# Kernel tuning notes

Hardware: AMD Instinct MI355X
Metric: run time of the kernel (lower is better)

Reference implementation:

```python
import jax, jax.numpy as jnp
import numpy as np

B, S, D, H = 2, 2048, 2048, 16
HD = D // H  # head_dim = 128


def setup_inputs() -> dict:
    key = jax.random.key(0)
    ks = jax.random.split(key, 9)
    std = 0.02
    x = jax.random.normal(ks[0], (B, S, D), dtype=jnp.float32)
    Wq = jax.random.normal(ks[1], (D, D), dtype=jnp.float32) * std
    bq = jnp.zeros((D,), dtype=jnp.float32)
    Wk = jax.random.normal(ks[2], (D, D), dtype=jnp.float32) * std
    bk = jnp.zeros((D,), dtype=jnp.float32)
    Wv = jax.random.normal(ks[3], (D, D), dtype=jnp.float32) * std
    bv = jnp.zeros((D,), dtype=jnp.float32)
    Wo = jax.random.normal(ks[4], (D, D), dtype=jnp.float32) * std
    bo = jnp.zeros((D,), dtype=jnp.float32)
    return {"x": x, "Wq": Wq, "bq": bq, "Wk": Wk, "bk": bk,
            "Wv": Wv, "bv": bv, "Wo": Wo, "bo": bo}


def _rope_tables(seq_len, head_dim, base=10000.0):
    # inv_freq over even indices; freqs: [S, HD/2]
    inv_freq = 1.0 / (base ** (jnp.arange(0, head_dim, 2, dtype=jnp.float32) / head_dim))
    t = jnp.arange(seq_len, dtype=jnp.float32)
    freqs = jnp.einsum('i,j->ij', t, inv_freq)
    return jnp.cos(freqs), jnp.sin(freqs)  # each [S, HD/2]


def _rotate(x, cos, sin):
    # x: [B, H, S, HD]; cos/sin: [S, HD/2] broadcast over B,H
    x1, x2 = jnp.split(x, 2, axis=-1)
    return jnp.concatenate([x1 * cos - x2 * sin, x1 * sin + x2 * cos], axis=-1)


def reference(x, Wq, bq, Wk, bk, Wv, bv, Wo, bo):
    b, s, d = x.shape
    q = (jnp.einsum('bsd,df->bsf', x, Wq) + bq).reshape(b, s, H, HD).transpose(0, 2, 1, 3)
    k = (jnp.einsum('bsd,df->bsf', x, Wk) + bk).reshape(b, s, H, HD).transpose(0, 2, 1, 3)
    v = (jnp.einsum('bsd,df->bsf', x, Wv) + bv).reshape(b, s, H, HD).transpose(0, 2, 1, 3)
    cos, sin = _rope_tables(s, HD)
    qr = _rotate(q, cos, sin)
    kr = _rotate(k, cos, sin)
    scores = jnp.einsum('bhqd,bhkd->bhqk', qr, kr) / jnp.sqrt(jnp.float32(HD))
    probs = jax.nn.softmax(scores, axis=-1)
    out = jnp.einsum('bhqk,bhkd->bhqd', probs, v)
    out = out.transpose(0, 2, 1, 3).reshape(b, s, d)
    return jnp.einsum('bsd,df->bsf', out, Wo) + bo
```

## Files before the change

kernel.cpp:

```cpp
#include <hip/hip_runtime.h>

#define BB  2
#define SS  2048
#define DD  2048
#define HH  16
#define HDD 128
#define BSR 4096

using short8  = __attribute__((ext_vector_type(8))) short;
using floatx4 = __attribute__((ext_vector_type(4))) float;

__device__ __forceinline__ float bf2f(unsigned short u) {
  return __uint_as_float(((unsigned int)u) << 16);
}
__device__ __forceinline__ unsigned short f2bf(float f) {
  unsigned int u = __float_as_uint(f);
  u += 0x7fffu + ((u >> 16) & 1u);
  return (unsigned short)(u >> 16);
}
__device__ __forceinline__ unsigned int pk2bf(float a, float b) {
  unsigned int ua = __float_as_uint(a);
  ua += 0x7fffu + ((ua >> 16) & 1u);
  unsigned int ub = __float_as_uint(b);
  ub += 0x7fffu + ((ub >> 16) & 1u);
  return (ua >> 16) | (ub & 0xffff0000u);
}
__device__ __forceinline__ void gl_lds16(const void* g, void* l) {
  __builtin_amdgcn_global_load_lds(
      (__attribute__((address_space(1))) void*)g,
      (__attribute__((address_space(3))) void*)l, 16, 0, 0);
}

__global__ __launch_bounds__(256) void transpose_w(
    const float* __restrict__ Wq, const float* __restrict__ Wk,
    const float* __restrict__ Wv, const float* __restrict__ Wo,
    unsigned short* __restrict__ wqkvt, unsigned short* __restrict__ wot)
{
  __shared__ float tile[32][33];
  const float* W; unsigned short* Out;
  int z = blockIdx.z;
  if      (z == 0) { W = Wq; Out = wqkvt; }
  else if (z == 1) { W = Wk; Out = wqkvt + (size_t)DD * DD; }
  else if (z == 2) { W = Wv; Out = wqkvt + 2 * (size_t)DD * DD; }
  else             { W = Wo; Out = wot; }
  int tx = threadIdx.x, ty = threadIdx.y;
  int d0 = blockIdx.y * 32, f0 = blockIdx.x * 32;
#pragma unroll
  for (int i = 0; i < 4; i++)
    tile[ty + i * 8][tx] = W[(size_t)(d0 + ty + i * 8) * DD + f0 + tx];
  __syncthreads();
#pragma unroll
  for (int i = 0; i < 4; i++)
    Out[(size_t)(f0 + ty + i * 8) * DD + d0 + tx] = f2bf(tile[tx][ty + i * 8]);
}

__global__ __launch_bounds__(256) void conv_x(const float* __restrict__ x,
                                              unsigned short* __restrict__ xb)
{
  size_t i = ((size_t)blockIdx.x * 256 + threadIdx.x) * 4;
  float4 v = *(const float4*)(x + i);
  ushort4 o;
  o.x = f2bf(v.x); o.y = f2bf(v.y); o.z = f2bf(v.z); o.w = f2bf(v.w);
  *(ushort4*)(xb + i) = o;
}

template <bool OUTF32>
__global__ __launch_bounds__(256) void gemm_bt(
    const unsigned short* __restrict__ A, const unsigned short* __restrict__ Bt,
    const float* __restrict__ bias, void* __restrict__ Cout,
    int M, int N, int K)
{
  __shared__ unsigned short As[128 * 64];
  __shared__ unsigned short Bs[128 * 64];
  int t = threadIdx.x;
  int m0 = blockIdx.y * 128, n0 = blockIdx.x * 128;
  int w = t >> 6, lane = t & 63, qd = lane >> 4, l16 = lane & 15;
  int wm = (w >> 1) * 64, wn = (w & 1) * 64;
  floatx4 zero4 = {0.f, 0.f, 0.f, 0.f};
  floatx4 acc[4][4];
#pragma unroll
  for (int i = 0; i < 4; i++)
#pragma unroll
    for (int j = 0; j < 4; j++) acc[i][j] = zero4;

  int gchunk = (t & 7) ^ ((t >> 3) & 7);
  const unsigned short* Ab = A  + (size_t)(m0 + (t >> 3)) * K + gchunk * 8;
  const unsigned short* Bb = Bt + (size_t)(n0 + (t >> 3)) * K + gchunk * 8;
  size_t qK = (size_t)32 * K;

  for (int k0 = 0; k0 < K; k0 += 64) {
    __syncthreads();
#pragma unroll
    for (int c = 0; c < 4; c++) {
      gl_lds16(Ab + c * qK + k0, &As[(c * 256 + t) * 8]);
      gl_lds16(Bb + c * qK + k0, &Bs[(c * 256 + t) * 8]);
    }
    __syncthreads();
#pragma unroll
    for (int ks = 0; ks < 2; ks++) {
      int ch = ((ks * 4 + qd) ^ (l16 & 7)) * 8;
      short8 af[4], bfr[4];
#pragma unroll
      for (int i = 0; i < 4; i++)
        af[i] = *(const short8*)&As[(wm + i * 16 + l16) * 64 + ch];
#pragma unroll
      for (int j = 0; j < 4; j++)
        bfr[j] = *(const short8*)&Bs[(wn + j * 16 + l16) * 64 + ch];
#pragma unroll
      for (int i = 0; i < 4; i++)
#pragma unroll
        for (int j = 0; j < 4; j++)
          acc[i][j] = __builtin_amdgcn_mfma_f32_16x16x32_bf16(af[i], bfr[j], acc[i][j], 0, 0, 0);
    }
  }

#pragma unroll
  for (int i = 0; i < 4; i++)
#pragma unroll
    for (int j = 0; j < 4; j++) {
      int row = m0 + wm + i * 16 + qd * 4;
      int col = n0 + wn + j * 16 + l16;
      float bsv = bias ? bias[col] : 0.f;
#pragma unroll
      for (int r = 0; r < 4; r++) {
        float v = acc[i][j][r] + bsv;
        if (OUTF32) ((float*)Cout)[(size_t)(row + r) * N + col] = v;
        else ((unsigned short*)Cout)[(size_t)(row + r) * N + col] = f2bf(v);
      }
    }
}

__global__ __launch_bounds__(256) void rope_qk(
    const unsigned short* __restrict__ qkv, const float* __restrict__ bq,
    const float* __restrict__ bk, unsigned short* __restrict__ q_r,
    unsigned short* __restrict__ k_r)
{
  int lin = blockIdx.x * 256 + threadIdx.x;
  int i = lin & 63;
  int s = (lin >> 6) & (SS - 1);
  int h = (lin >> 17) & (HH - 1);
  int b = lin >> 21;
  size_t row = (size_t)(b * SS + s) * (3 * DD);
  int f = h * HDD + i;
  float q1 = bf2f(qkv[row + f])            + bq[f];
  float q2 = bf2f(qkv[row + f + 64])       + bq[f + 64];
  float k1 = bf2f(qkv[row + DD + f])       + bk[f];
  float k2 = bf2f(qkv[row + DD + f + 64])  + bk[f + 64];
  float inv = powf(10000.f, -(float)i * (1.f / 64.f));
  float ang = (float)s * inv;
  float sn, c;
  sincosf(ang, &sn, &c);
  const float qs = 0.08838834764831845f;
  size_t ob = ((size_t)(b * HH + h) * SS + s) * HDD;
  q_r[ob + i]      = f2bf((q1 * c - q2 * sn) * qs);
  q_r[ob + i + 64] = f2bf((q1 * sn + q2 * c) * qs);
  k_r[ob + i]      = f2bf(k1 * c - k2 * sn);
  k_r[ob + i + 64] = f2bf(k1 * sn + k2 * c);
}

__global__ __launch_bounds__(256) void v_transpose(
    const unsigned short* __restrict__ qkv, const float* __restrict__ bv,
    unsigned short* __restrict__ v_t)
{
  __shared__ float tile[32][33];
  int bh = blockIdx.z; int b = bh >> 4, h = bh & 15;
  int s0 = blockIdx.x * 32, d0 = blockIdx.y * 32;
  int tx = threadIdx.x, ty = threadIdx.y;
#pragma unroll
  for (int i = 0; i < 4; i++) {
    int s = s0 + ty + i * 8, dh = d0 + tx;
    tile[ty + i * 8][tx] =
        bf2f(qkv[(size_t)(b * SS + s) * (3 * DD) + 2 * DD + h * HDD + dh]) + bv[h * HDD + dh];
  }
  __syncthreads();
  int s = s0 + tx;
  int y = s & 63;
  int kap = ((y >> 5) & 1) * 32 + ((y >> 2) & 3) * 8 + ((y >> 4) & 1) * 4 + (y & 3);
  int scol = (s & ~63) + kap;
#pragma unroll
  for (int i = 0; i < 4; i++)
    v_t[((size_t)(b * HH + h) * HDD + d0 + ty + i * 8) * SS + scol] =
        f2bf(tile[tx][ty + i * 8]);
}

__global__ __launch_bounds__(256, 2) void attn_kernel(
    const unsigned short* __restrict__ q_r, const unsigned short* __restrict__ k_r,
    const unsigned short* __restrict__ v_t, unsigned short* __restrict__ aout)
{
  __shared__ unsigned short Ks[2][64 * 128];
  __shared__ unsigned short Vs[2][128 * 64];
  int t = threadIdx.x, w = t >> 6, lane = t & 63, qd = lane >> 4, l16 = lane & 15;
  int L = blockIdx.y * gridDim.x + blockIdx.x;
  int jj = L >> 3;
  int bh = (L & 7) * 4 + (jj >> 4);
  int q0 = (jj & 15) * 128;
  const unsigned short* qb = q_r + (size_t)bh * SS * HDD;
  const unsigned short* kb = k_r + (size_t)bh * SS * HDD;
  const unsigned short* vb = v_t + (size_t)bh * HDD * SS;

  short8 aq[2][4];
#pragma unroll
  for (int mi = 0; mi < 2; mi++)
#pragma unroll
    for (int ks = 0; ks < 4; ks++)
      aq[mi][ks] = *(const short8*)
          &qb[(size_t)(q0 + w * 32 + mi * 16 + l16) * HDD + ks * 32 + qd * 8];

  float m_i[2], l_i[2];
  floatx4 zero4 = {0.f, 0.f, 0.f, 0.f};
  floatx4 o[2][8];
#pragma unroll
  for (int mi = 0; mi < 2; mi++) { m_i[mi] = -1e30f; l_i[mi] = 0.f; }
#pragma unroll
  for (int mi = 0; mi < 2; mi++)
#pragma unroll
    for (int n = 0; n < 8; n++) o[mi][n] = zero4;

  auto stage = [&](int nb, int kt) {
#pragma unroll
    for (int c = 0; c < 4; c++) {
      int flat = c * 256 + t;
      int r = flat >> 4, cc = flat & 15;
      gl_lds16(kb + (size_t)(kt + r) * HDD + (cc ^ (r & 15)) * 8, &Ks[nb][flat * 8]);
    }
#pragma unroll
    for (int c = 0; c < 4; c++) {
      int flat = c * 256 + t;
      int r = flat >> 3, cc = flat & 7;
      gl_lds16(vb + (size_t)r * SS + kt + (cc ^ (r & 7)) * 8, &Vs[nb][flat * 8]);
    }
  };

  stage(0, 0);
  int buf = 0;

  for (int kt = 0; kt < SS; kt += 64) {
    __syncthreads();
    if (kt + 64 < SS) stage(buf ^ 1, kt + 64);

    floatx4 sc[2][4];
#pragma unroll
    for (int mi = 0; mi < 2; mi++)
#pragma unroll
      for (int j = 0; j < 4; j++) sc[mi][j] = zero4;
#pragma unroll
    for (int j = 0; j < 4; j++) {
      int krow = j * 16 + l16;
#pragma unroll
      for (int ks = 0; ks < 4; ks++) {
        int chunk = ks * 4 + qd;
        short8 kf = *(const short8*)&Ks[buf][krow * 128 + ((chunk ^ (krow & 15)) * 8)];
        sc[0][j] = __builtin_amdgcn_mfma_f32_16x16x32_bf16(kf, aq[0][ks], sc[0][j], 0, 0, 0);
        sc[1][j] = __builtin_amdgcn_mfma_f32_16x16x32_bf16(kf, aq[1][ks], sc[1][j], 0, 0, 0);
      }
    }

    float rmax[2];
#pragma unroll
    for (int mi = 0; mi < 2; mi++) {
      float m = sc[mi][0][0];
#pragma unroll
      for (int j = 0; j < 4; j++)
#pragma unroll
        for (int r = 0; r < 4; r++) m = fmaxf(m, sc[mi][j][r]);
      m = fmaxf(m, __shfl_xor(m, 16, 64));
      m = fmaxf(m, __shfl_xor(m, 32, 64));
      rmax[mi] = m;
    }

    bool up = (rmax[0] > m_i[0]) || (rmax[1] > m_i[1]);
    if (__ballot(up) != 0ull) {
#pragma unroll
      for (int mi = 0; mi < 2; mi++) {
        float mn = fmaxf(m_i[mi], rmax[mi]);
        float a = __expf(m_i[mi] - mn);
        m_i[mi] = mn;
        l_i[mi] *= a;
#pragma unroll
        for (int n = 0; n < 8; n++)
#pragma unroll
          for (int r = 0; r < 4; r++) o[mi][n][r] *= a;
      }
    }

    unsigned int pr[2][4][2];
#pragma unroll
    for (int mi = 0; mi < 2; mi++) {
      float s0 = 0.f;
#pragma unroll
      for (int j = 0; j < 4; j++) {
        float p0 = __expf(sc[mi][j][0] - m_i[mi]);
        float p1 = __expf(sc[mi][j][1] - m_i[mi]);
        float p2 = __expf(sc[mi][j][2] - m_i[mi]);
        float p3 = __expf(sc[mi][j][3] - m_i[mi]);
        s0 += (p0 + p1) + (p2 + p3);
        pr[mi][j][0] = pk2bf(p0, p1);
        pr[mi][j][1] = pk2bf(p2, p3);
      }
      s0 += __shfl_xor(s0, 16, 64);
      s0 += __shfl_xor(s0, 32, 64);
      l_i[mi] += s0;
    }

#pragma unroll
    for (int n = 0; n < 8; n++) {
      int vrow = n * 16 + l16;
#pragma unroll
      for (int ks = 0; ks < 2; ks++) {
        int chunk = ks * 4 + qd;
        short8 av = *(const short8*)&Vs[buf][vrow * 64 + ((chunk ^ (vrow & 7)) * 8)];
        union { unsigned int u[4]; short8 v; } bp0, bp1;
        bp0.u[0] = pr[0][2 * ks][0];     bp0.u[1] = pr[0][2 * ks][1];
        bp0.u[2] = pr[0][2 * ks + 1][0]; bp0.u[3] = pr[0][2 * ks + 1][1];
        bp1.u[0] = pr[1][2 * ks][0];     bp1.u[1] = pr[1][2 * ks][1];
        bp1.u[2] = pr[1][2 * ks + 1][0]; bp1.u[3] = pr[1][2 * ks + 1][1];
        o[0][n] = __builtin_amdgcn_mfma_f32_16x16x32_bf16(av, bp0.v, o[0][n], 0, 0, 0);
        o[1][n] = __builtin_amdgcn_mfma_f32_16x16x32_bf16(av, bp1.v, o[1][n], 0, 0, 0);
      }
    }
    buf ^= 1;
  }

  int b = bh >> 4, h = bh & 15;
#pragma unroll
  for (int mi = 0; mi < 2; mi++) {
    int qrow = q0 + w * 32 + mi * 16 + l16;
    float inv_l = 1.f / l_i[mi];
    size_t base = ((size_t)(b * SS + qrow)) * DD + h * HDD;
#pragma unroll
    for (int n = 0; n < 8; n++) {
      uint2 pkd;
      pkd.x = pk2bf(o[mi][n][0] * inv_l, o[mi][n][1] * inv_l);
      pkd.y = pk2bf(o[mi][n][2] * inv_l, o[mi][n][3] * inv_l);
      *(uint2*)&aout[base + n * 16 + qd * 4] = pkd;
    }
  }
}

extern "C" void kernel_launch(void* const* d_in, const int* in_sizes, int n_in,
                              void* d_out, int out_size, void* d_ws, size_t ws_size,
                              hipStream_t stream) {
  const float* x  = (const float*)d_in[0];
  const float* Wq = (const float*)d_in[1];
  const float* bq = (const float*)d_in[2];
  const float* Wk = (const float*)d_in[3];
  const float* bk = (const float*)d_in[4];
  const float* Wv = (const float*)d_in[5];
  const float* bv = (const float*)d_in[6];
  const float* Wo = (const float*)d_in[7];
  const float* bo = (const float*)d_in[8];
  float* out = (float*)d_out;

  char* ws = (char*)d_ws;
  unsigned short* xb      = (unsigned short*)(ws + 0);
  unsigned short* wqkvt   = (unsigned short*)(ws + 16777216);
  unsigned short* wot     = (unsigned short*)(ws + 41943040);
  unsigned short* qkv     = (unsigned short*)(ws + 50331648);
  unsigned short* q_r     = (unsigned short*)(ws + 100663296);
  unsigned short* k_r     = (unsigned short*)(ws + 117440512);
  unsigned short* v_t     = (unsigned short*)(ws + 134217728);
  unsigned short* attn_o  = xb;

  transpose_w<<<dim3(DD / 32, DD / 32, 4), dim3(32, 8), 0, stream>>>(
      Wq, Wk, Wv, Wo, wqkvt, wot);
  conv_x<<<dim3((BSR * DD) / 1024), dim3(256), 0, stream>>>(x, xb);
  gemm_bt<false><<<dim3(3 * DD / 128, BSR / 128), dim3(256), 0, stream>>>(
      xb, wqkvt, nullptr, qkv, BSR, 3 * DD, DD);
  rope_qk<<<dim3((BB * HH * SS * 64) / 256), dim3(256), 0, stream>>>(
      qkv, bq, bk, q_r, k_r);
  v_transpose<<<dim3(SS / 32, HDD / 32, BB * HH), dim3(32, 8), 0, stream>>>(
      qkv, bv, v_t);
  attn_kernel<<<dim3(SS / 128, BB * HH), dim3(256), 0, stream>>>(
      q_r, k_r, v_t, attn_o);
  gemm_bt<true><<<dim3(DD / 128, BSR / 128), dim3(256), 0, stream>>>(
      attn_o, wot, bo, out, BSR, DD, DD);
}
```

Measured before the change: 443.7 us.

## Fuse bias, RoPE and V transpose into QKV GEMM epilogue; use exp2 in softmax

Adds a gemm_qkv kernel whose epilogue stages the output tile in LDS, adds the bias, applies RoPE from a precomputed cos/sin table, and writes Q/K in head-major layout and V transposed. This removes the bf16 qkv intermediate round-trip and the separate rope_qk and v_transpose kernels. The Q scale is changed to fold log2(e), and the attention softmax uses the native exp2 builtin instead of __expf, which saves a multiply per exponent. The fused epilogue adds LDS traffic and a bf16 rounding step before RoPE, and it depends on the log2e folding being consistent.

```diff
diff --git a/kernel.cpp b/kernel.cpp
--- a/kernel.cpp
+++ b/kernel.cpp
@@ -24,6 +24,13 @@
   unsigned int ub = __float_as_uint(b);
   ub += 0x7fffu + ((ub >> 16) & 1u);
   return (ua >> 16) | (ub & 0xffff0000u);
+}
+__device__ __forceinline__ float fexp2(float x) {
+#if __has_builtin(__builtin_amdgcn_exp2f)
+  return __builtin_amdgcn_exp2f(x);
+#else
+  return __expf(x * 0.6931471805599453f);
+#endif
 }
 __device__ __forceinline__ void gl_lds16(const void* g, void* l) {
   __builtin_amdgcn_global_load_lds(
@@ -64,6 +71,124 @@
   *(ushort4*)(xb + i) = o;
 }
 
+__global__ __launch_bounds__(256) void rope_tab(float2* __restrict__ rtab) {
+  int idx = blockIdx.x * 256 + threadIdx.x;
+  int s = idx >> 6, c = idx & 63;
+  float inv = powf(10000.f, -(float)c * (1.f / 64.f));
+  float ang = (float)s * inv;
+  float sn, cc;
+  sincosf(ang, &sn, &cc);
+  rtab[idx] = make_float2(cc, sn);
+}
+
+__global__ __launch_bounds__(256) void gemm_qkv(
+    const unsigned short* __restrict__ A, const unsigned short* __restrict__ Bt,
+    const float* __restrict__ bq, const float* __restrict__ bk,
+    const float* __restrict__ bv, const float2* __restrict__ rtab,
+    unsigned short* __restrict__ q_r, unsigned short* __restrict__ k_r,
+    unsigned short* __restrict__ v_t)
+{
+  __shared__ unsigned short smem[16896];
+  unsigned short* As = smem;
+  unsigned short* Bs = smem + 8192;
+  const int K = DD;
+  int t = threadIdx.x;
+  int m0 = blockIdx.y * 128, n0 = blockIdx.x * 128;
+  int w = t >> 6, lane = t & 63, qd = lane >> 4, l16 = lane & 15;
+  int wm = (w >> 1) * 64, wn = (w & 1) * 64;
+  floatx4 zero4 = {0.f, 0.f, 0.f, 0.f};
+  floatx4 acc[4][4];
+#pragma unroll
+  for (int i = 0; i < 4; i++)
+#pragma unroll
+    for (int j = 0; j < 4; j++) acc[i][j] = zero4;
+
+  int gchunk = (t & 7) ^ ((t >> 3) & 7);
+  const unsigned short* Ab = A  + (size_t)(m0 + (t >> 3)) * K + gchunk * 8;
+  const unsigned short* Bb = Bt + (size_t)(n0 + (t >> 3)) * K + gchunk * 8;
+  size_t qK = (size_t)32 * K;
+
+  for (int k0 = 0; k0 < K; k0 += 64) {
+    __syncthreads();
+#pragma unroll
+    for (int c = 0; c < 4; c++) {
+      gl_lds16(Ab + c * qK + k0, &As[(c * 256 + t) * 8]);
+      gl_lds16(Bb + c * qK + k0, &Bs[(c * 256 + t) * 8]);
+    }
+    __syncthreads();
+#pragma unroll
+    for (int ks = 0; ks < 2; ks++) {
+      int ch = ((ks * 4 + qd) ^ (l16 & 7)) * 8;
+      short8 af[4], bfr[4];
+#pragma unroll
+      for (int i = 0; i < 4; i++)
+        af[i] = *(const short8*)&As[(wm + i * 16 + l16) * 64 + ch];
+#pragma unroll
+      for (int j = 0; j < 4; j++)
+        bfr[j] = *(const short8*)&Bs[(wn + j * 16 + l16) * 64 + ch];
+#pragma unroll
+      for (int i = 0; i < 4; i++)
+#pragma unroll
+        for (int j = 0; j < 4; j++)
+          acc[i][j] = __builtin_amdgcn_mfma_f32_16x16x32_bf16(af[i], bfr[j], acc[i][j], 0, 0, 0);
+    }
+  }
+
+  int plane = n0 >> 11;
+  int h = (n0 >> 7) & 15;
+  const float* bias = plane == 0 ? bq : (plane == 1 ? bk : bv);
+  __syncthreads();
+#pragma unroll
+  for (int i = 0; i < 4; i++)
+#pragma unroll
+    for (int j = 0; j < 4; j++) {
+      int rl = wm + i * 16 + qd * 4;
+      int cl = wn + j * 16 + l16;
+      float bsv = bias[h * 128 + cl];
+#pragma unroll
+      for (int r = 0; r < 4; r++)
+        smem[(rl + r) * 132 + cl] = f2bf(acc[i][j][r] + bsv);
+    }
+  __syncthreads();
+
+  int b = m0 >> 11, sbase = m0 & (SS - 1);
+  if (plane < 2) {
+    unsigned short* dst = (plane == 0 ? q_r : k_r) + (size_t)(b * HH + h) * SS * HDD;
+    const float fac = (plane == 0) ? 0.12751744f : 1.0f;
+#pragma unroll
+    for (int it = 0; it < 16; it++) {
+      int idx = it * 256 + t;
+      int rl = idx >> 5, c2 = (idx & 31) * 2;
+      int s = sbase + rl;
+      float4 cs = *(const float4*)&rtab[(size_t)s * 64 + c2];
+      float a0 = bf2f(smem[rl * 132 + c2]);
+      float a1 = bf2f(smem[rl * 132 + c2 + 1]);
+      float b0 = bf2f(smem[rl * 132 + c2 + 64]);
+      float b1 = bf2f(smem[rl * 132 + c2 + 65]);
+      unsigned int lo = pk2bf((a0 * cs.x - b0 * cs.y) * fac,
+                              (a1 * cs.z - b1 * cs.w) * fac);
+      unsigned int hi = pk2bf((a0 * cs.y + b0 * cs.x) * fac,
+                              (a1 * cs.w + b1 * cs.z) * fac);
+      size_t rowb = (size_t)s * HDD;
+      *(unsigned int*)&dst[rowb + c2]      = lo;
+      *(unsigned int*)&dst[rowb + c2 + 64] = hi;
+    }
+  } else {
+    unsigned short* dst = v_t + (size_t)(b * HH + h) * HDD * SS;
+#pragma unroll
+    for (int it = 0; it < 32; it++) {
+      int idx = it * 256 + t;
+      int hd = idx >> 6, sp = (idx & 63) * 2;
+      unsigned short v0 = smem[sp * 132 + hd];
+      unsigned short v1 = smem[(sp + 1) * 132 + hd];
+      int y = sp & 63;
+      int kap = ((y >> 5) & 1) * 32 + ((y >> 2) & 3) * 8 + ((y >> 4) & 1) * 4 + (y & 3);
+      int sg = sbase + (sp & ~63) + kap;
+      *(unsigned int*)&dst[(size_t)hd * SS + sg] = ((unsigned int)v1 << 16) | v0;
+    }
+  }
+}
+
 template <bool OUTF32>
 __global__ __launch_bounds__(256) void gemm_bt(
     const unsigned short* __restrict__ A, const unsigned short* __restrict__ Bt,
@@ -130,59 +255,6 @@
     }
 }
 
-__global__ __launch_bounds__(256) void rope_qk(
-    const unsigned short* __restrict__ qkv, const float* __restrict__ bq,
-    const float* __restrict__ bk, unsigned short* __restrict__ q_r,
-    unsigned short* __restrict__ k_r)
-{
-  int lin = blockIdx.x * 256 + threadIdx.x;
-  int i = lin & 63;
-  int s = (lin >> 6) & (SS - 1);
-  int h = (lin >> 17) & (HH - 1);
-  int b = lin >> 21;
-  size_t row = (size_t)(b * SS + s) * (3 * DD);
-  int f = h * HDD + i;
-  float q1 = bf2f(qkv[row + f])            + bq[f];
-  float q2 = bf2f(qkv[row + f + 64])       + bq[f + 64];
-  float k1 = bf2f(qkv[row + DD + f])       + bk[f];
-  float k2 = bf2f(qkv[row + DD + f + 64])  + bk[f + 64];
-  float inv = powf(10000.f, -(float)i * (1.f / 64.f));
-  float ang = (float)s * inv;
-  float sn, c;
-  sincosf(ang, &sn, &c);
-  const float qs = 0.08838834764831845f;
-  size_t ob = ((size_t)(b * HH + h) * SS + s) * HDD;
-  q_r[ob + i]      = f2bf((q1 * c - q2 * sn) * qs);
-  q_r[ob + i + 64] = f2bf((q1 * sn + q2 * c) * qs);
-  k_r[ob + i]      = f2bf(k1 * c - k2 * sn);
-  k_r[ob + i + 64] = f2bf(k1 * sn + k2 * c);
-}
-
-__global__ __launch_bounds__(256) void v_transpose(
-    const unsigned short* __restrict__ qkv, const float* __restrict__ bv,
-    unsigned short* __restrict__ v_t)
-{
-  __shared__ float tile[32][33];
-  int bh = blockIdx.z; int b = bh >> 4, h = bh & 15;
-  int s0 = blockIdx.x * 32, d0 = blockIdx.y * 32;
-  int tx = threadIdx.x, ty = threadIdx.y;
-#pragma unroll
-  for (int i = 0; i < 4; i++) {
-    int s = s0 + ty + i * 8, dh = d0 + tx;
-    tile[ty + i * 8][tx] =
-        bf2f(qkv[(size_t)(b * SS + s) * (3 * DD) + 2 * DD + h * HDD + dh]) + bv[h * HDD + dh];
-  }
-  __syncthreads();
-  int s = s0 + tx;
-  int y = s & 63;
-  int kap = ((y >> 5) & 1) * 32 + ((y >> 2) & 3) * 8 + ((y >> 4) & 1) * 4 + (y & 3);
-  int scol = (s & ~63) + kap;
-#pragma unroll
-  for (int i = 0; i < 4; i++)
-    v_t[((size_t)(b * HH + h) * HDD + d0 + ty + i * 8) * SS + scol] =
-        f2bf(tile[tx][ty + i * 8]);
-}
-
 __global__ __launch_bounds__(256, 2) void attn_kernel(
     const unsigned short* __restrict__ q_r, const unsigned short* __restrict__ k_r,
     const unsigned short* __restrict__ v_t, unsigned short* __restrict__ aout)
@@ -273,7 +345,7 @@
 #pragma unroll
       for (int mi = 0; mi < 2; mi++) {
         float mn = fmaxf(m_i[mi], rmax[mi]);
-        float a = __expf(m_i[mi] - mn);
+        float a = fexp2(m_i[mi] - mn);
         m_i[mi] = mn;
         l_i[mi] *= a;
 #pragma unroll
@@ -289,10 +361,10 @@
       float s0 = 0.f;
 #pragma unroll
       for (int j = 0; j < 4; j++) {
-        float p0 = __expf(sc[mi][j][0] - m_i[mi]);
-        float p1 = __expf(sc[mi][j][1] - m_i[mi]);
-        float p2 = __expf(sc[mi][j][2] - m_i[mi]);
-        float p3 = __expf(sc[mi][j][3] - m_i[mi]);
+        float p0 = fexp2(sc[mi][j][0] - m_i[mi]);
+        float p1 = fexp2(sc[mi][j][1] - m_i[mi]);
+        float p2 = fexp2(sc[mi][j][2] - m_i[mi]);
+        float p3 = fexp2(sc[mi][j][3] - m_i[mi]);
         s0 += (p0 + p1) + (p2 + p3);
         pr[mi][j][0] = pk2bf(p0, p1);
         pr[mi][j][1] = pk2bf(p2, p3);
@@ -355,7 +427,7 @@
   unsigned short* xb      = (unsigned short*)(ws + 0);
   unsigned short* wqkvt   = (unsigned short*)(ws + 16777216);
   unsigned short* wot     = (unsigned short*)(ws + 41943040);
-  unsigned short* qkv     = (unsigned short*)(ws + 50331648);
+  float2*         rtab    = (float2*)(ws + 50331648);
   unsigned short* q_r     = (unsigned short*)(ws + 100663296);
   unsigned short* k_r     = (unsigned short*)(ws + 117440512);
   unsigned short* v_t     = (unsigned short*)(ws + 134217728);
@@ -364,12 +436,9 @@
   transpose_w<<<dim3(DD / 32, DD / 32, 4), dim3(32, 8), 0, stream>>>(
       Wq, Wk, Wv, Wo, wqkvt, wot);
   conv_x<<<dim3((BSR * DD) / 1024), dim3(256), 0, stream>>>(x, xb);
-  gemm_bt<false><<<dim3(3 * DD / 128, BSR / 128), dim3(256), 0, stream>>>(
-      xb, wqkvt, nullptr, qkv, BSR, 3 * DD, DD);
-  rope_qk<<<dim3((BB * HH * SS * 64) / 256), dim3(256), 0, stream>>>(
-      qkv, bq, bk, q_r, k_r);
-  v_transpose<<<dim3(SS / 32, HDD / 32, BB * HH), dim3(32, 8), 0, stream>>>(
-      qkv, bv, v_t);
+  rope_tab<<<dim3((SS * 64) / 256), dim3(256), 0, stream>>>(rtab);
+  gemm_qkv<<<dim3(3 * DD / 128, BSR / 128), dim3(256), 0, stream>>>(
+      xb, wqkvt, bq, bk, bv, rtab, q_r, k_r, v_t);
   attn_kernel<<<dim3(SS / 128, BB * HH), dim3(256), 0, stream>>>(
       q_r, k_r, v_t, attn_o);
   gemm_bt<true><<<dim3(DD / 128, BSR / 128), dim3(256), 0, stream>>>(
```

Measured after the change: 395.4 us. -10.9%, faster.
